# Kernel tuning notes

Hardware: AMD Instinct MI355X
Metric: run time of the kernel (lower is better)

## Reference

```python
import jax, jax.numpy as jnp
import numpy as np

N_HEAD, D_MODEL, D_K, D_V = 8, 512, 64, 64
WINDOW, THRESH = 2, 0.5
TEMP = float(np.sqrt(D_K))
LN_EPS = 1e-5


def setup_inputs() -> dict:
    key = jax.random.key(0)
    ks = jax.random.split(key, 12)
    B, L = 4, 2048
    std_qk = np.sqrt(2.0 / (D_MODEL + D_K))
    std_v = np.sqrt(2.0 / (D_MODEL + D_V))
    return {
        "q": jax.random.normal(ks[0], (B, L, D_MODEL), jnp.float32),
        "k": jax.random.normal(ks[1], (B, L, D_MODEL), jnp.float32),
        "v": jax.random.normal(ks[2], (B, L, D_MODEL), jnp.float32),
        "w_q": jax.random.normal(ks[3], (N_HEAD * D_K, D_MODEL), jnp.float32) * std_qk,
        "b_q": jnp.zeros((N_HEAD * D_K,), jnp.float32),
        "w_k": jax.random.normal(ks[4], (N_HEAD * D_K, D_MODEL), jnp.float32) * std_qk,
        "b_k": jnp.zeros((N_HEAD * D_K,), jnp.float32),
        "w_v": jax.random.normal(ks[5], (N_HEAD * D_V, D_MODEL), jnp.float32) * std_v,
        "b_v": jnp.zeros((N_HEAD * D_V,), jnp.float32),
        "w_g": jax.random.normal(ks[6], (1, D_K), jnp.float32) * (1.0 / np.sqrt(D_K)),
        "b_g": jnp.zeros((1,), jnp.float32),
        "w_fc": jax.random.normal(ks[7], (D_MODEL, N_HEAD * D_V), jnp.float32) * (1.0 / np.sqrt(D_MODEL)),
        "b_fc": jnp.zeros((D_MODEL,), jnp.float32),
        "ln_g": jnp.ones((D_MODEL,), jnp.float32),
        "ln_b": jnp.zeros((D_MODEL,), jnp.float32),
    }


def reference(q, k, v, w_q, b_q, w_k, b_k, w_v, b_v, w_g, b_g, w_fc, b_fc, ln_g, ln_b):
    B, Lq, _ = q.shape
    Lk = k.shape[1]
    residual = q
    # project and split heads: (h, B, L, d)
    qh = (q @ w_q.T + b_q).reshape(B, Lq, N_HEAD, D_K).transpose(2, 0, 1, 3)
    kh = (k @ w_k.T + b_k).reshape(B, Lk, N_HEAD, D_K).transpose(2, 0, 1, 3)
    vh = (v @ w_v.T + b_v).reshape(B, Lk, N_HEAD, D_V).transpose(2, 0, 1, 3)

    scores = jnp.einsum('hbqd,hbkd->hbqk', qh, kh) / TEMP  # (h, B, Lq, Lk)

    # dynamic gate: tokens with sigmoid(gate) > THRESH keep full attention,
    # others are restricted to a +/-WINDOW sliding window
    gate_open = jax.nn.sigmoid(jnp.einsum('hbqd,od->hbqo', qh, w_g) + b_g)[..., 0] > THRESH
    i = jnp.arange(Lq)[:, None]
    j = jnp.arange(Lk)[None, :]
    win = jnp.abs(i - j) <= WINDOW  # (Lq, Lk)
    allowed = gate_open[..., None] | win  # (h, B, Lq, Lk)
    scores = jnp.where(allowed, scores, -jnp.inf)

    attn = jax.nn.softmax(scores, axis=-1)  # dropout is identity in eval
    out = jnp.einsum('hbqk,hbkd->hbqd', attn, vh)
    out = out.transpose(1, 2, 0, 3).reshape(B, Lq, N_HEAD * D_V)
    out = out @ w_fc.T + b_fc

    x = out + residual
    mu = jnp.mean(x, axis=-1, keepdims=True)
    var = jnp.mean((x - mu) ** 2, axis=-1, keepdims=True)
    out = (x - mu) * jax.lax.rsqrt(var + LN_EPS) * ln_g + ln_b

    return out, attn.reshape(N_HEAD * B, Lq, Lk)
```

## Files before the change

kernel.cpp:

```cpp
#include <hip/hip_runtime.h>


typedef _Float16 f16;
typedef _Float16 f16x8 __attribute__((ext_vector_type(8)));
typedef _Float16 f16x4 __attribute__((ext_vector_type(4)));
typedef float f32x4 __attribute__((ext_vector_type(4)));

#define OUT0_ELEMS (4 * 2048 * 512)

__device__ __forceinline__ f16x8 cvt8(float4 a, float4 b) {
  f16x8 r;
  r[0] = (f16)a.x; r[1] = (f16)a.y; r[2] = (f16)a.z; r[3] = (f16)a.w;
  r[4] = (f16)b.x; r[5] = (f16)b.y; r[6] = (f16)b.z; r[7] = (f16)b.w;
  return r;
}

__device__ __forceinline__ void bar_lds() {
  asm volatile("s_waitcnt lgkmcnt(0)" ::: "memory");
  __builtin_amdgcn_s_barrier();
}

__global__ __launch_bounds__(256) void prep_kernel(
    const float* __restrict__ w_q, const float* __restrict__ b_q,
    const float* __restrict__ w_g, const float* __restrict__ b_g,
    double* __restrict__ wge, double* __restrict__ bqg) {
  int idx = blockIdx.x * 256 + threadIdx.x;
  if (idx < 4096) {
    int h = idx >> 9, c = idx & 511;
    double acc = 0.0;
    for (int d = 0; d < 64; ++d)
      acc += (double)w_g[d] * (double)w_q[(h * 64 + d) * 512 + c];
    wge[idx] = acc;
  }
  if (idx < 8) {
    double acc = (double)b_g[0];
    for (int d = 0; d < 64; ++d)
      acc += (double)b_q[idx * 64 + d] * (double)w_g[d];
    bqg[idx] = acc;
  }
}

__global__ __launch_bounds__(256) void gate_kernel(
    const float* __restrict__ q, const double* __restrict__ wge,
    const double* __restrict__ bqg, int* __restrict__ gate) {
  int lane = threadIdx.x & 63, wid = threadIdx.x >> 6;
  int tok = blockIdx.x * 4 + wid;
  int b = tok >> 11, l = tok & 2047;
  const float* qr = q + (long)tok * 512;
  float qv[8];
#pragma unroll
  for (int j = 0; j < 8; ++j) qv[j] = qr[lane + 64 * j];
#pragma unroll
  for (int h = 0; h < 8; ++h) {
    double acc = 0.0;
#pragma unroll
    for (int j = 0; j < 8; ++j) acc += (double)qv[j] * wge[h * 512 + lane + 64 * j];
#pragma unroll
    for (int off = 1; off < 64; off <<= 1) acc += __shfl_xor(acc, off);
    double logit = acc + bqg[h];
    if (lane == 0) gate[(h * 4 + b) * 2048 + l] = (logit > 0.0) ? 1 : 0;
  }
}

__global__ __launch_bounds__(256) void compact_kernel(
    const int* __restrict__ gate, unsigned short* __restrict__ perm,
    int* __restrict__ nopen) {
  __shared__ int wsum[4];
  const int hb = blockIdx.x, t = threadIdx.x;
  const int lane = t & 63, wid = t >> 6;
  const int base = hb * 2048;
  int g[8];
  int cnt = 0;
#pragma unroll
  for (int i = 0; i < 8; ++i) { g[i] = gate[base + t * 8 + i]; cnt += g[i]; }
  int inc = cnt;
#pragma unroll
  for (int off = 1; off < 64; off <<= 1) {
    int y = __shfl_up(inc, off);
    if (lane >= off) inc += y;
  }
  if (lane == 63) wsum[wid] = inc;
  __syncthreads();
  int wbase = 0;
  for (int w = 0; w < wid; ++w) wbase += wsum[w];
  const int totOpen = wsum[0] + wsum[1] + wsum[2] + wsum[3];
  int openPos = wbase + inc - cnt;
  int closedPos = totOpen + t * 8 - openPos;
#pragma unroll
  for (int i = 0; i < 8; ++i) {
    int l = t * 8 + i;
    if (g[i]) perm[base + openPos++] = (unsigned short)l;
    else      perm[base + closedPos++] = (unsigned short)l;
  }
  if (t == 0) nopen[hb] = totOpen;
}

template <int EPI>
__global__ __launch_bounds__(256) void gemm512(
    const float* __restrict__ A, const float* __restrict__ W,
    const float* __restrict__ bias, const float* __restrict__ res,
    f16* __restrict__ out16, float* __restrict__ outf) {
  __shared__ __align__(16) f16 As[64 * 32];
  __shared__ __align__(16) f16 Ws[64 * 32];
  const int tid = threadIdx.x;
  const int lane = tid & 63, wid = tid >> 6;
  const int lo = lane & 15, hi = lane >> 4;
  const int m0 = blockIdx.x * 64, n0 = blockIdx.y * 64;
  const int wm = wid >> 1, wn = wid & 1;

  const int srow = tid >> 2, sseg = tid & 3;
  const int ssu = sseg ^ (srow & 3);
  const float* gA = A + (long)(m0 + srow) * 512 + sseg * 8;
  const float* gW = W + (long)(n0 + srow) * 512 + sseg * 8;
  f16* wA = &As[srow * 32 + ssu * 8];
  f16* wW = &Ws[srow * 32 + ssu * 8];

  const f32x4 zero4 = {0.f, 0.f, 0.f, 0.f};
  f32x4 acc[2][2] = {{zero4, zero4}, {zero4, zero4}};
  const int ra0 = wm * 32 + lo;
  const int rb0 = wn * 32 + lo;
  const int sa = hi ^ (ra0 & 3);
  const int sb = hi ^ (rb0 & 3);

  for (int kk = 0; kk < 512; kk += 32) {
    float4 a0 = *(const float4*)(gA + kk);
    float4 a1 = *(const float4*)(gA + kk + 4);
    float4 w0 = *(const float4*)(gW + kk);
    float4 w1 = *(const float4*)(gW + kk + 4);
    *(f16x8*)wA = cvt8(a0, a1);
    *(f16x8*)wW = cvt8(w0, w1);
    __syncthreads();
    f16x8 af0 = *(const f16x8*)&As[ra0 * 32 + sa * 8];
    f16x8 af1 = *(const f16x8*)&As[(ra0 + 16) * 32 + sa * 8];
    f16x8 bf0 = *(const f16x8*)&Ws[rb0 * 32 + sb * 8];
    f16x8 bf1 = *(const f16x8*)&Ws[(rb0 + 16) * 32 + sb * 8];
    acc[0][0] = __builtin_amdgcn_mfma_f32_16x16x32_f16(af0, bf0, acc[0][0], 0, 0, 0);
    acc[0][1] = __builtin_amdgcn_mfma_f32_16x16x32_f16(af0, bf1, acc[0][1], 0, 0, 0);
    acc[1][0] = __builtin_amdgcn_mfma_f32_16x16x32_f16(af1, bf0, acc[1][0], 0, 0, 0);
    acc[1][1] = __builtin_amdgcn_mfma_f32_16x16x32_f16(af1, bf1, acc[1][1], 0, 0, 0);
    __syncthreads();
  }

#pragma unroll
  for (int i = 0; i < 2; ++i)
#pragma unroll
    for (int j = 0; j < 2; ++j)
#pragma unroll
      for (int r = 0; r < 4; ++r) {
        const int m = m0 + wm * 32 + i * 16 + hi * 4 + r;
        const int n = n0 + wn * 32 + j * 16 + lo;
        float v = acc[i][j][r] + bias[n];
        if constexpr (EPI == 0) {
          const int b = m >> 11, l = m & 2047, h = n >> 6, d = n & 63;
          out16[(long)((h * 4 + b) * 2048 + l) * 64 + d] = (f16)v;
        } else if constexpr (EPI == 2) {
          const int b = m >> 11, l = m & 2047, h = n >> 6, d = n & 63;
          out16[(long)((h * 4 + b) * 64 + d) * 2048 + l] = (f16)v;
        } else {
          outf[(long)m * 512 + n] = v + res[(long)m * 512 + n];
        }
      }
}

__device__ __forceinline__ uint4 ldK512(const f16* __restrict__ g, int tid) {
  return *(const uint4*)(g + tid * 8);
}
__device__ __forceinline__ uint4 ldV512(const f16* __restrict__ g, int tid) {
  return *(const uint4*)(g + (long)(tid >> 3) * 2048 + ((tid & 7) << 3));
}
__device__ __forceinline__ void stW512(uint4 s, f16* lds, int tid) {
  const int row = tid >> 3, seg = tid & 7, sw = row & 7;
  *(uint4*)&lds[(row << 6) + ((seg ^ sw) << 3)] = s;
}

__global__ __launch_bounds__(512) void attn_kernel(
    const f16* __restrict__ qh, const f16* __restrict__ kh,
    const f16* __restrict__ vt, const int* __restrict__ gate,
    const unsigned short* __restrict__ perm, const int* __restrict__ nopen,
    float* __restrict__ attn, float* __restrict__ o) {
  __shared__ __align__(16) f16 Ks[2][4096];
  __shared__ __align__(16) f16 Vs[2][4096];
  __shared__ __align__(16) f16 Ps[8][1024];
  const int tid = threadIdx.x;
  const int lane = tid & 63, wid = tid >> 6;
  const int bid = blockIdx.x;

  if (bid >= 512) {
    const int vb = bid - 512;
    const int xcd = vb & 7, sub = vb >> 3;
    const int hb = xcd * 4 + (sub >> 5);
    const int chunk = sub & 31;
    const int nop = nopen[hb];
    const int j0 = ((nop + 127) & ~127) + (chunk << 6);
    if (j0 >= 2048) return;
    unsigned short* rowIdx = (unsigned short*)&Ks[0][0];
    if (tid < 64) rowIdx[tid] = perm[hb * 2048 + j0 + tid];
    __syncthreads();
    float* abase = attn + ((long)hb * 2048 << 11);
    const f32x4 zero4 = {0.f, 0.f, 0.f, 0.f};
    for (int it = 0; it < 64; ++it)
      *(f32x4*)(abase + ((long)rowIdx[it] << 11) + (tid << 2)) = zero4;
    __syncthreads();
    const f16* qhb = qh + (long)hb * 2048 * 64;
    const f16* khb = kh + (long)hb * 2048 * 64;
    const f16* vtb = vt + (long)hb * 64 * 2048;
    const int b = hb & 3, h = hb >> 2;
    for (int rr = 0; rr < 8; ++rr) {
      const int row = rowIdx[(wid << 3) + rr];
      const int jlo = max(row - 2, 0), jhi = min(row + 2, 2047);
      const float qv = (float)qhb[(long)row * 64 + lane];
      float p0, p1, p2, p3, p4, sum = 0.f;
#pragma unroll
      for (int jj = 0; jj < 5; ++jj) {
        const int j = jlo + jj;
        const int js = min(j, 2047);
        float prod = qv * (float)khb[(long)js * 64 + lane];
        prod += __shfl_xor(prod, 1);
        prod += __shfl_xor(prod, 2);
        prod += __shfl_xor(prod, 4);
        prod += __shfl_xor(prod, 8);
        prod += __shfl_xor(prod, 16);
        prod += __shfl_xor(prod, 32);
        const float e = (j <= jhi) ? __expf(prod * 0.125f) : 0.f;
        if (jj == 0) p0 = e; else if (jj == 1) p1 = e; else if (jj == 2) p2 = e;
        else if (jj == 3) p3 = e; else p4 = e;
        sum += e;
      }
      const float inv = 1.f / sum;
      float pv = p0;
      pv = (lane == 1) ? p1 : pv;
      pv = (lane == 2) ? p2 : pv;
      pv = (lane == 3) ? p3 : pv;
      pv = (lane == 4) ? p4 : pv;
      if (lane < 5 && (jlo + lane) <= jhi)
        abase[((long)row << 11) + jlo + lane] = pv * inv;
      float od = 0.f;
      od += p0 * (float)vtb[(long)lane * 2048 + min(jlo + 0, 2047)];
      od += p1 * (float)vtb[(long)lane * 2048 + min(jlo + 1, 2047)];
      od += p2 * (float)vtb[(long)lane * 2048 + min(jlo + 2, 2047)];
      od += p3 * (float)vtb[(long)lane * 2048 + min(jlo + 3, 2047)];
      od += p4 * (float)vtb[(long)lane * 2048 + min(jlo + 4, 2047)];
      o[(long)(b * 2048 + row) * 512 + (h << 6) + lane] = od * inv;
    }
    return;
  }

  const int lo = lane & 15, hi = lane >> 4;
  const int xcd = bid & 7, local = bid >> 3;
  const int hb = xcd * 4 + (local >> 4);
  const int q0 = (local & 15) << 7;
  const int nop = nopen[hb];
  if (q0 >= nop) return;

  const unsigned short* pm = perm + hb * 2048 + q0;
  const f16* khb = kh + (long)hb * 2048 * 64;
  const f16* vtb = vt + (long)hb * 64 * 2048;

  const int rowA = pm[(wid << 4) + lo];
  const f16* qrow = qh + (long)(hb * 2048 + rowA) * 64;
  const f16x8 aq0 = *(const f16x8*)(qrow + (hi << 3));
  const f16x8 aq1 = *(const f16x8*)(qrow + 32 + (hi << 3));

  int qi[4], gt[4];
  float psum[4];
#pragma unroll
  for (int r = 0; r < 4; ++r) {
    qi[r] = pm[(wid << 4) + (hi << 2) + r];
    gt[r] = gate[hb * 2048 + qi[r]];
    psum[r] = 0.f;
  }
  const f32x4 zero4 = {0.f, 0.f, 0.f, 0.f};

  {
    uint4 kreg = ldK512(khb, tid);
    stW512(kreg, &Ks[0][0], tid);
    kreg = ldK512(khb + 4096, tid);
    int cur = 0;
    for (int kt = 0; kt < 32; ++kt) {
      bar_lds();
      if (kt < 31) {
        stW512(kreg, &Ks[cur ^ 1][0], tid);
        if (kt < 30) kreg = ldK512(khb + (long)(kt + 2) * 4096, tid);
      }
      const f16* Kc = &Ks[cur][0];
      f32x4 sacc[4] = {zero4, zero4, zero4, zero4};
      __builtin_amdgcn_s_setprio(1);
#pragma unroll
      for (int s = 0; s < 2; ++s) {
        const f16x8 a = s ? aq1 : aq0;
#pragma unroll
        for (int nt = 0; nt < 4; ++nt) {
          const int krow = (nt << 4) + lo;
          const f16x8 b = *(const f16x8*)&Kc[(krow << 6) + ((((s << 2) + hi) ^ (krow & 7)) << 3)];
          sacc[nt] = __builtin_amdgcn_mfma_f32_16x16x32_f16(a, b, sacc[nt], 0, 0, 0);
        }
      }
      __builtin_amdgcn_s_setprio(0);
      const int kkb = (kt << 6) + lo;
#pragma unroll
      for (int nt = 0; nt < 4; ++nt) {
        const int kk = kkb + (nt << 4);
#pragma unroll
        for (int r = 0; r < 4; ++r) {
          const bool allowed = gt[r] || ((unsigned)(kk - qi[r] + 2) <= 4u);
          psum[r] += allowed ? __expf(sacc[nt][r] * 0.125f) : 0.f;
        }
      }
      cur ^= 1;
    }
  }

  float invl[4];
#pragma unroll
  for (int r = 0; r < 4; ++r) {
    float s = psum[r];
    s += __shfl_xor(s, 1);
    s += __shfl_xor(s, 2);
    s += __shfl_xor(s, 4);
    s += __shfl_xor(s, 8);
    invl[r] = 1.f / s;
  }

  f32x4 oacc[4] = {zero4, zero4, zero4, zero4};
  f16* Pw = &Ps[wid][0];
  const int row2 = lane >> 2, qq = lane & 3;
  float* arow = attn + ((long)(hb * 2048 + pm[(wid << 4) + row2]) << 11);

  {
    uint4 kreg = ldK512(khb, tid);
    uint4 vreg = ldV512(vtb, tid);
    stW512(kreg, &Ks[0][0], tid);
    stW512(vreg, &Vs[0][0], tid);
    kreg = ldK512(khb + 4096, tid);
    vreg = ldV512(vtb + 64, tid);
    int cur = 0;
    for (int kt = 0; kt < 32; ++kt) {
      bar_lds();
      if (kt < 31) {
        stW512(kreg, &Ks[cur ^ 1][0], tid);
        stW512(vreg, &Vs[cur ^ 1][0], tid);
        if (kt < 30) {
          kreg = ldK512(khb + (long)(kt + 2) * 4096, tid);
          vreg = ldV512(vtb + ((kt + 2) << 6), tid);
        }
      }
      const f16* Kc = &Ks[cur][0];
      const f16* Vc = &Vs[cur][0];
      f32x4 sacc[4] = {zero4, zero4, zero4, zero4};
      __builtin_amdgcn_s_setprio(1);
#pragma unroll
      for (int s = 0; s < 2; ++s) {
        const f16x8 a = s ? aq1 : aq0;
#pragma unroll
        for (int nt = 0; nt < 4; ++nt) {
          const int krow = (nt << 4) + lo;
          const f16x8 b = *(const f16x8*)&Kc[(krow << 6) + ((((s << 2) + hi) ^ (krow & 7)) << 3)];
          sacc[nt] = __builtin_amdgcn_mfma_f32_16x16x32_f16(a, b, sacc[nt], 0, 0, 0);
        }
      }
      __builtin_amdgcn_s_setprio(0);
      const int kkb = (kt << 6) + lo;
#pragma unroll
      for (int nt = 0; nt < 4; ++nt) {
        const int kk = kkb + (nt << 4);
#pragma unroll
        for (int r = 0; r < 4; ++r) {
          const bool allowed = gt[r] || ((unsigned)(kk - qi[r] + 2) <= 4u);
          const float p = allowed ? __expf(sacc[nt][r] * 0.125f) * invl[r] : 0.f;
          const int prow = (hi << 2) + r;
          const int pcol = (nt << 4) + lo;
          Pw[(prow << 6) + (((pcol >> 3) ^ (prow & 7)) << 3) + (pcol & 7)] = (f16)p;
        }
      }
      __builtin_amdgcn_s_setprio(1);
#pragma unroll
      for (int s = 0; s < 2; ++s) {
        const f16x8 ap = *(const f16x8*)&Pw[(lo << 6) + ((((s << 2) + hi) ^ (lo & 7)) << 3)];
#pragma unroll
        for (int nt = 0; nt < 4; ++nt) {
          const int vrow = (nt << 4) + lo;
          const f16x8 bv = *(const f16x8*)&Vc[(vrow << 6) + ((((s << 2) + hi) ^ (vrow & 7)) << 3)];
          oacc[nt] = __builtin_amdgcn_mfma_f32_16x16x32_f16(ap, bv, oacc[nt], 0, 0, 0);
        }
      }
      __builtin_amdgcn_s_setprio(0);
      {
        const int swz = row2 & 7;
        float* dst = arow + (kt << 6) + (qq << 2);
#pragma unroll
        for (int i = 0; i < 4; ++i) {
          const f16x4 pv = *(const f16x4*)&Pw[(row2 << 6) + ((((i << 1) + (qq >> 1)) ^ swz) << 3) + ((qq & 1) << 2)];
          f32x4 fo = {(float)pv[0], (float)pv[1], (float)pv[2], (float)pv[3]};
          *(f32x4*)(dst + (i << 4)) = fo;
        }
      }
      cur ^= 1;
    }
  }

  const int b = hb & 3, h = hb >> 2;
#pragma unroll
  for (int nt = 0; nt < 4; ++nt)
#pragma unroll
    for (int r = 0; r < 4; ++r)
      o[(long)(b * 2048 + qi[r]) * 512 + (h << 6) + (nt << 4) + lo] = oacc[nt][r];
}

__global__ __launch_bounds__(256) void ln_kernel(float* __restrict__ x,
                                                 const float* __restrict__ g,
                                                 const float* __restrict__ bta) {
  __shared__ float red[8];
  const int t = threadIdx.x;
  float* row = x + (long)blockIdx.x * 512;
  float v0 = row[t], v1 = row[t + 256];
  float s = v0 + v1;
#pragma unroll
  for (int off = 1; off < 64; off <<= 1) s += __shfl_xor(s, off);
  if ((t & 63) == 0) red[t >> 6] = s;
  __syncthreads();
  const float mean = (red[0] + red[1] + red[2] + red[3]) * (1.f / 512.f);
  const float d0 = v0 - mean, d1 = v1 - mean;
  float sq = d0 * d0 + d1 * d1;
#pragma unroll
  for (int off = 1; off < 64; off <<= 1) sq += __shfl_xor(sq, off);
  if ((t & 63) == 0) red[4 + (t >> 6)] = sq;
  __syncthreads();
  const float var = (red[4] + red[5] + red[6] + red[7]) * (1.f / 512.f);
  const float rstd = 1.f / sqrtf(var + 1e-5f);
  row[t] = d0 * rstd * g[t] + bta[t];
  row[t + 256] = d1 * rstd * g[t + 256] + bta[t + 256];
}

extern "C" void kernel_launch(void* const* d_in, const int* in_sizes, int n_in,
                              void* d_out, int out_size, void* d_ws, size_t ws_size,
                              hipStream_t stream) {
  const float* q    = (const float*)d_in[0];
  const float* k    = (const float*)d_in[1];
  const float* v    = (const float*)d_in[2];
  const float* w_q  = (const float*)d_in[3];
  const float* b_q  = (const float*)d_in[4];
  const float* w_k  = (const float*)d_in[5];
  const float* b_k  = (const float*)d_in[6];
  const float* w_v  = (const float*)d_in[7];
  const float* b_v  = (const float*)d_in[8];
  const float* w_g  = (const float*)d_in[9];
  const float* b_g  = (const float*)d_in[10];
  const float* w_fc = (const float*)d_in[11];
  const float* b_fc = (const float*)d_in[12];
  const float* ln_g = (const float*)d_in[13];
  const float* ln_b = (const float*)d_in[14];

  char* wsb = (char*)d_ws;
  f16* qh16   = (f16*)wsb;
  f16* kh16   = qh16 + 4194304;
  f16* vt16   = kh16 + 4194304;
  float* ob   = (float*)(wsb + 25165824);
  int* gateb  = (int*)(wsb + 25165824 + 16777216);
  double* wge = (double*)(wsb + 25165824 + 16777216 + 262144);
  double* bqg = wge + 4096;
  unsigned short* permb = (unsigned short*)(wsb + 25165824 + 16777216 + 262144 + 32768 + 64);
  int* nopenb = (int*)(wsb + 25165824 + 16777216 + 262144 + 32768 + 64 + 131072);

  float* out0 = (float*)d_out;
  float* attn = out0 + OUT0_ELEMS;

  prep_kernel<<<16, 256, 0, stream>>>(w_q, b_q, w_g, b_g, wge, bqg);
  gate_kernel<<<2048, 256, 0, stream>>>(q, wge, bqg, gateb);
  compact_kernel<<<32, 256, 0, stream>>>(gateb, permb, nopenb);

  dim3 gp(128, 8);
  gemm512<0><<<gp, 256, 0, stream>>>(q, w_q, b_q, nullptr, qh16, nullptr);
  gemm512<0><<<gp, 256, 0, stream>>>(k, w_k, b_k, nullptr, kh16, nullptr);
  gemm512<2><<<gp, 256, 0, stream>>>(v, w_v, b_v, nullptr, vt16, nullptr);

  attn_kernel<<<1536, 512, 0, stream>>>(qh16, kh16, vt16, gateb, permb, nopenb, attn, ob);

  gemm512<3><<<gp, 256, 0, stream>>>(ob, w_fc, b_fc, q, nullptr, out0);
  ln_kernel<<<8192, 256, 0, stream>>>(out0, ln_g, ln_b);
}
```

Before: 269.6 us.

## Double-buffer projection GEMM tiles and interleave attention block types

The projection GEMM now keeps two LDS stages and issues the global loads for the next K slice before the barrier and MFMAs of the current one. This removes one barrier per iteration and overlaps load latency with compute. The attention launch also changes its block-id mapping so heavy gated blocks and light windowed/zeroing blocks alternate in a 1:2 pattern instead of sitting in two contiguous ranges. The aim is better load balance across CUs, at the cost of some integer div/mod overhead and an untested remapping that must still cover all 512+1024 blocks exactly once.

```diff
diff --git a/kernel.cpp b/kernel.cpp
--- a/kernel.cpp
+++ b/kernel.cpp
@@ -100,8 +100,8 @@
     const float* __restrict__ A, const float* __restrict__ W,
     const float* __restrict__ bias, const float* __restrict__ res,
     f16* __restrict__ out16, float* __restrict__ outf) {
-  __shared__ __align__(16) f16 As[64 * 32];
-  __shared__ __align__(16) f16 Ws[64 * 32];
+  __shared__ __align__(16) f16 As[2][64 * 32];
+  __shared__ __align__(16) f16 Ws[2][64 * 32];
   const int tid = threadIdx.x;
   const int lane = tid & 63, wid = tid >> 6;
   const int lo = lane & 15, hi = lane >> 4;
@@ -112,8 +112,7 @@
   const int ssu = sseg ^ (srow & 3);
   const float* gA = A + (long)(m0 + srow) * 512 + sseg * 8;
   const float* gW = W + (long)(n0 + srow) * 512 + sseg * 8;
-  f16* wA = &As[srow * 32 + ssu * 8];
-  f16* wW = &Ws[srow * 32 + ssu * 8];
+  const int wofs = srow * 32 + ssu * 8;
 
   const f32x4 zero4 = {0.f, 0.f, 0.f, 0.f};
   f32x4 acc[2][2] = {{zero4, zero4}, {zero4, zero4}};
@@ -122,23 +121,30 @@
   const int sa = hi ^ (ra0 & 3);
   const int sb = hi ^ (rb0 & 3);
 
-  for (int kk = 0; kk < 512; kk += 32) {
-    float4 a0 = *(const float4*)(gA + kk);
-    float4 a1 = *(const float4*)(gA + kk + 4);
-    float4 w0 = *(const float4*)(gW + kk);
-    float4 w1 = *(const float4*)(gW + kk + 4);
-    *(f16x8*)wA = cvt8(a0, a1);
-    *(f16x8*)wW = cvt8(w0, w1);
-    __syncthreads();
-    f16x8 af0 = *(const f16x8*)&As[ra0 * 32 + sa * 8];
-    f16x8 af1 = *(const f16x8*)&As[(ra0 + 16) * 32 + sa * 8];
-    f16x8 bf0 = *(const f16x8*)&Ws[rb0 * 32 + sb * 8];
-    f16x8 bf1 = *(const f16x8*)&Ws[(rb0 + 16) * 32 + sb * 8];
+  float4 a0 = *(const float4*)(gA);
+  float4 a1 = *(const float4*)(gA + 4);
+  float4 w0 = *(const float4*)(gW);
+  float4 w1 = *(const float4*)(gW + 4);
+  int cur = 0;
+  for (int kk = 0; kk < 16; ++kk) {
+    *(f16x8*)&As[cur][wofs] = cvt8(a0, a1);
+    *(f16x8*)&Ws[cur][wofs] = cvt8(w0, w1);
+    if (kk < 15) {
+      const float* pA = gA + (kk + 1) * 32;
+      const float* pW = gW + (kk + 1) * 32;
+      a0 = *(const float4*)pA; a1 = *(const float4*)(pA + 4);
+      w0 = *(const float4*)pW; w1 = *(const float4*)(pW + 4);
+    }
+    bar_lds();
+    f16x8 af0 = *(const f16x8*)&As[cur][ra0 * 32 + sa * 8];
+    f16x8 af1 = *(const f16x8*)&As[cur][(ra0 + 16) * 32 + sa * 8];
+    f16x8 bf0 = *(const f16x8*)&Ws[cur][rb0 * 32 + sb * 8];
+    f16x8 bf1 = *(const f16x8*)&Ws[cur][(rb0 + 16) * 32 + sb * 8];
     acc[0][0] = __builtin_amdgcn_mfma_f32_16x16x32_f16(af0, bf0, acc[0][0], 0, 0, 0);
     acc[0][1] = __builtin_amdgcn_mfma_f32_16x16x32_f16(af0, bf1, acc[0][1], 0, 0, 0);
     acc[1][0] = __builtin_amdgcn_mfma_f32_16x16x32_f16(af1, bf0, acc[1][0], 0, 0, 0);
     acc[1][1] = __builtin_amdgcn_mfma_f32_16x16x32_f16(af1, bf1, acc[1][1], 0, 0, 0);
-    __syncthreads();
+    cur ^= 1;
   }
 
 #pragma unroll
@@ -184,12 +190,13 @@
   const int tid = threadIdx.x;
   const int lane = tid & 63, wid = tid >> 6;
   const int bid = blockIdx.x;
-
-  if (bid >= 512) {
-    const int vb = bid - 512;
-    const int xcd = vb & 7, sub = vb >> 3;
-    const int hb = xcd * 4 + (sub >> 5);
-    const int chunk = sub & 31;
+  const int xcd = bid & 7;
+  const int sq = bid >> 3;
+
+  if (sq % 3 != 0) {
+    const int vb = sq - sq / 3 - 1;
+    const int hb = xcd * 4 + (vb >> 5);
+    const int chunk = vb & 31;
     const int nop = nopen[hb];
     const int j0 = ((nop + 127) & ~127) + (chunk << 6);
     if (j0 >= 2048) return;
@@ -246,9 +253,9 @@
   }
 
   const int lo = lane & 15, hi = lane >> 4;
-  const int xcd = bid & 7, local = bid >> 3;
-  const int hb = xcd * 4 + (local >> 4);
-  const int q0 = (local & 15) << 7;
+  const int a = sq / 3;
+  const int hb = xcd * 4 + (a >> 4);
+  const int q0 = (a & 15) << 7;
   const int nop = nopen[hb];
   if (q0 >= nop) return;
 
@@ -287,12 +294,12 @@
       __builtin_amdgcn_s_setprio(1);
 #pragma unroll
       for (int s = 0; s < 2; ++s) {
-        const f16x8 a = s ? aq1 : aq0;
+        const f16x8 aa = s ? aq1 : aq0;
 #pragma unroll
         for (int nt = 0; nt < 4; ++nt) {
           const int krow = (nt << 4) + lo;
           const f16x8 b = *(const f16x8*)&Kc[(krow << 6) + ((((s << 2) + hi) ^ (krow & 7)) << 3)];
-          sacc[nt] = __builtin_amdgcn_mfma_f32_16x16x32_f16(a, b, sacc[nt], 0, 0, 0);
+          sacc[nt] = __builtin_amdgcn_mfma_f32_16x16x32_f16(aa, b, sacc[nt], 0, 0, 0);
         }
       }
       __builtin_amdgcn_s_setprio(0);
@@ -350,12 +357,12 @@
       __builtin_amdgcn_s_setprio(1);
 #pragma unroll
       for (int s = 0; s < 2; ++s) {
-        const f16x8 a = s ? aq1 : aq0;
+        const f16x8 aa = s ? aq1 : aq0;
 #pragma unroll
         for (int nt = 0; nt < 4; ++nt) {
           const int krow = (nt << 4) + lo;
           const f16x8 b = *(const f16x8*)&Kc[(krow << 6) + ((((s << 2) + hi) ^ (krow & 7)) << 3)];
-          sacc[nt] = __builtin_amdgcn_mfma_f32_16x16x32_f16(a, b, sacc[nt], 0, 0, 0);
+          sacc[nt] = __builtin_amdgcn_mfma_f32_16x16x32_f16(aa, b, sacc[nt], 0, 0, 0);
         }
       }
       __builtin_amdgcn_s_setprio(0);
```

After: 307.0 us. +13.9%, slower.
